# Performance work log

Hardware: AMD Instinct MI355X
Metric: run time of the kernel (lower is better)

The kernel has to match this reference:

```python
import jax, jax.numpy as jnp
import numpy as np

CHEB_K = 2  # Chebyshev polynomial order (init arg cheb_k)


def _avwgcn(x, E, w_pool, b_pool):
    """Adaptive Vertex-Wise Graph Convolution (AGCRN's AVWGCN).
    x: [B, N, C_in], E: [N, D], w_pool: [D, K, C_in, C_out], b_pool: [D, C_out].
    """
    N = E.shape[0]
    # adaptive adjacency from node embeddings
    supports = jax.nn.softmax(jax.nn.relu(E @ E.T), axis=1)  # [N, N]
    support_set = [jnp.eye(N, dtype=x.dtype), supports]
    for _ in range(2, CHEB_K):
        support_set.append(2.0 * supports @ support_set[-1] - support_set[-2])
    supports_k = jnp.stack(support_set)  # [K, N, N]
    # per-node adaptive weights/bias generated from embeddings
    weights = jnp.einsum('nd,dkio->nkio', E, w_pool)  # [N, K, C_in, C_out]
    bias = E @ b_pool  # [N, C_out]
    # graph propagation then per-node adaptive projection
    x_g = jnp.einsum('knm,bmc->bnkc', supports_k, x)  # [B, N, K, C_in]
    return jnp.einsum('bnki,nkio->bno', x_g, weights) + bias  # [B, N, C_out]


def setup_inputs() -> dict:
    key = jax.random.key(0)
    ks = jax.random.split(key, 7)
    B, N, DIN, DOUT, D = 64, 2048, 2, 64, 10
    return {
        'x': jax.random.normal(ks[0], (B, N, DIN), dtype=jnp.float32),
        'state': jax.random.normal(ks[1], (B, N, DOUT), dtype=jnp.float32),
        'node_embeddings': jax.random.normal(ks[2], (N, D), dtype=jnp.float32),
        'gate_w_pool': jax.random.normal(ks[3], (D, CHEB_K, DIN + DOUT, 2 * DOUT), dtype=jnp.float32) * 0.1,
        'gate_b_pool': jax.random.normal(ks[4], (D, 2 * DOUT), dtype=jnp.float32) * 0.1,
        'update_w_pool': jax.random.normal(ks[5], (D, CHEB_K, DIN + DOUT, DOUT), dtype=jnp.float32) * 0.1,
        'update_b_pool': jax.random.normal(ks[6], (D, DOUT), dtype=jnp.float32) * 0.1,
    }


def reference(x, state, node_embeddings, gate_w_pool, gate_b_pool, update_w_pool, update_b_pool):
    hidden_dim = state.shape[-1]
    input_and_state = jnp.concatenate([x, state], axis=-1)  # [B, N, DIN+DOUT]
    z_r = jax.nn.sigmoid(_avwgcn(input_and_state, node_embeddings, gate_w_pool, gate_b_pool))
    z, r = z_r[..., :hidden_dim], z_r[..., hidden_dim:]
    candidate = jnp.concatenate([x, z * state], axis=-1)
    hc = jnp.tanh(_avwgcn(candidate, node_embeddings, update_w_pool, update_b_pool))
    h = r * state + (1.0 - r) * hc
    return h
```

## Files before the change

### kernel.cpp

```cpp
#include <hip/hip_runtime.h>
#include <math.h>

#define N_NODES 2048
#define BATCH   64
#define DIN     2
#define DOUT    64
#define CIN     66
#define CP      68
#define D_EMB   10
#define GOUT    128
#define NCOLS   (BATCH*CP)
#define MK      2048
#define KTOT    132
#define KPAD    136

typedef __attribute__((ext_vector_type(8))) short bf16x8;
typedef __attribute__((ext_vector_type(8))) unsigned short u16x8;
typedef __attribute__((ext_vector_type(4))) float f32x4;

__device__ __forceinline__ unsigned short f2bf_rn(float f) {
    unsigned u = __builtin_bit_cast(unsigned, f);
    unsigned r = u + 0x7FFFu + ((u >> 16) & 1u);
    return (unsigned short)(r >> 16);
}
__device__ __forceinline__ float bf2f(unsigned short h) {
    unsigned u = ((unsigned)h) << 16;
    return __builtin_bit_cast(float, u);
}

__device__ __forceinline__ void gload_lds16(const void* g, void* l) {
    __builtin_amdgcn_global_load_lds(
        (const __attribute__((address_space(1))) unsigned int*)g,
        (__attribute__((address_space(3))) unsigned int*)l, 16, 0, 0);
}

__device__ __forceinline__ int frag_addr(int strip, int kt, int row, int slice) {
    const int byte = ((strip * 5 + kt) * 16 + row) * 64 + slice * 16;
    return byte ^ ((row & 7) << 4);
}

__global__ __launch_bounds__(256) void transpose_pool_kernel(
    const float* __restrict__ wp, float* __restrict__ wpT, int OC, int total)
{
    const int idx = blockIdx.x * 256 + threadIdx.x;
    if (idx >= total) return;
    const int kp   = idx % KPAD;
    const int rest = idx / KPAD;
    const int o    = rest % OC;
    const int d    = rest / OC;
    wpT[idx] = (kp < KTOT) ? wp[((size_t)d * KTOT + kp) * OC + o] : 0.f;
}

__global__ __launch_bounds__(256) void supports_kernel(
    const float* __restrict__ E, unsigned short* __restrict__ S_hi)
{
    const int n   = blockIdx.x;
    const int tid = threadIdx.x;

    float en[D_EMB];
#pragma unroll
    for (int d = 0; d < D_EMB; ++d) en[d] = E[n * D_EMB + d];

    float vals[8];
    float mx = -1e30f;
#pragma unroll
    for (int j = 0; j < 8; ++j) {
        const int m = tid + j * 256;
        float dot = 0.f;
#pragma unroll
        for (int d = 0; d < D_EMB; ++d) dot += en[d] * E[m * D_EMB + d];
        dot = fmaxf(dot, 0.f);
        vals[j] = dot;
        mx = fmaxf(mx, dot);
    }

    __shared__ float sred[4];
    for (int off = 32; off > 0; off >>= 1) mx = fmaxf(mx, __shfl_xor(mx, off));
    if ((tid & 63) == 0) sred[tid >> 6] = mx;
    __syncthreads();
    mx = fmaxf(fmaxf(sred[0], sred[1]), fmaxf(sred[2], sred[3]));

    float sum = 0.f;
#pragma unroll
    for (int j = 0; j < 8; ++j) { vals[j] = __expf(vals[j] - mx); sum += vals[j]; }

    __syncthreads();
    for (int off = 32; off > 0; off >>= 1) sum += __shfl_xor(sum, off);
    if ((tid & 63) == 0) sred[tid >> 6] = sum;
    __syncthreads();
    sum = sred[0] + sred[1] + sred[2] + sred[3];

    const float inv = 1.f / sum;
#pragma unroll
    for (int j = 0; j < 8; ++j)
        S_hi[(size_t)n * N_NODES + tid + j * 256] = f2bf_rn(vals[j] * inv);
}

__global__ __launch_bounds__(256) void build_xt_kernel(
    const float* __restrict__ x, const float* __restrict__ state,
    const unsigned short* __restrict__ zs, const int use_zs,
    unsigned short* __restrict__ XT)
{
    const int b   = blockIdx.y;
    const int m0  = blockIdx.x * 64;
    const int tid = threadIdx.x;
    __shared__ float T[64][69];

    {
        const int r = tid >> 2;
        const int q = (tid & 3) * 16;
        if (use_zs) {
            const u16x8 v0 = *(const u16x8*)&zs[((size_t)(m0 + r) * BATCH + b) * DOUT + q];
            const u16x8 v1 = *(const u16x8*)&zs[((size_t)(m0 + r) * BATCH + b) * DOUT + q + 8];
#pragma unroll
            for (int u = 0; u < 8; ++u) {
                T[r][DIN + q + u]     = bf2f(v0[u]);
                T[r][DIN + q + 8 + u] = bf2f(v1[u]);
            }
        } else {
#pragma unroll
            for (int u = 0; u < 4; ++u) {
                const float4 v = *(const float4*)&state[((size_t)b * N_NODES + m0 + r) * DOUT + q + u * 4];
                T[r][DIN + q + u * 4 + 0] = v.x;
                T[r][DIN + q + u * 4 + 1] = v.y;
                T[r][DIN + q + u * 4 + 2] = v.z;
                T[r][DIN + q + u * 4 + 3] = v.w;
            }
        }
    }
    if (tid < 128) {
        const int r = tid >> 1, c = tid & 1;
        T[r][c] = x[((size_t)b * N_NODES + m0 + r) * DIN + c];
        T[r][CIN + c] = 0.f;
    }
    __syncthreads();

    for (int idx = tid; idx < CP * 64; idx += 256) {
        const int c  = idx >> 6;
        const int mm = idx & 63;
        XT[((size_t)(b * CP + c)) * N_NODES + m0 + mm] = f2bf_rn(T[mm][c]);
    }
}

__global__ __launch_bounds__(256) void gemm_mfma_kernel(
    const unsigned short* __restrict__ A,
    const unsigned short* __restrict__ BT, float* __restrict__ C)
{
    __shared__ __align__(16) unsigned short As[4096];
    __shared__ __align__(16) unsigned short Bs[4096];

    const int tid  = threadIdx.x;
    const int lane = tid & 63;
    const int w    = tid >> 6;
    const int wr   = w >> 1, wc = w & 1;

    const int wg   = blockIdx.x;
    const int wgid = (wg & 7) * 68 + (wg >> 3);
    const int bn   = wgid % 34;
    const int bm   = wgid / 34;

    f32x4 acc[4][4];
#pragma unroll
    for (int i = 0; i < 4; ++i)
#pragma unroll
        for (int j = 0; j < 4; ++j) acc[i][j] = (f32x4){0.f, 0.f, 0.f, 0.f};

    const int srow = ((tid >> 6) << 4) + (tid & 15);
    const int scol = ((tid >> 4) & 3) * 8;
    const unsigned a_off0 = (unsigned)(bm * 128 + srow) * MK + scol;
    const unsigned a_off1 = a_off0 + 64u * MK;
    const unsigned b_off0 = (unsigned)(bn * 128 + srow) * MK + scol;
    const unsigned b_off1 = b_off0 + 64u * MK;

    unsigned short* asl0 = As + tid * 8;
    unsigned short* asl1 = As + 2048 + tid * 8;
    unsigned short* bsl0 = Bs + tid * 8;
    unsigned short* bsl1 = Bs + 2048 + tid * 8;

#pragma unroll 1
    for (int k0 = 0; k0 < MK; k0 += 32) {
        gload_lds16(A  + a_off0 + k0, asl0);
        gload_lds16(A  + a_off1 + k0, asl1);
        gload_lds16(BT + b_off0 + k0, bsl0);
        gload_lds16(BT + b_off1 + k0, bsl1);
        __syncthreads();

        bf16x8 af[4], bf[4];
#pragma unroll
        for (int i = 0; i < 4; ++i)
            af[i] = *(const bf16x8*)(As + ((wr * 4 + i) * 64 + lane) * 8);
#pragma unroll
        for (int j = 0; j < 4; ++j)
            bf[j] = *(const bf16x8*)(Bs + ((wc * 4 + j) * 64 + lane) * 8);
#pragma unroll
        for (int i = 0; i < 4; ++i)
#pragma unroll
            for (int j = 0; j < 4; ++j)
                acc[i][j] = __builtin_amdgcn_mfma_f32_16x16x32_bf16(
                    af[i], bf[j], acc[i][j], 0, 0, 0);
        __syncthreads();
    }

    const int crow0 = bm * 128 + wr * 64;
    const int ccol0 = bn * 128 + wc * 64;
#pragma unroll
    for (int i = 0; i < 4; ++i)
#pragma unroll
        for (int j = 0; j < 4; ++j)
#pragma unroll
            for (int r = 0; r < 4; ++r) {
                const int row = crow0 + i * 16 + (lane >> 4) * 4 + r;
                const int col = ccol0 + j * 16 + (lane & 15);
                C[(size_t)row * NCOLS + col] = acc[i][j][r];
            }
}

__global__ __launch_bounds__(256) void gate_mfma_kernel(
    const float* __restrict__ E, const float* __restrict__ wpT,
    const float* __restrict__ bp, const float* __restrict__ x,
    const float* __restrict__ state, const float* __restrict__ AG,
    unsigned short* __restrict__ ZS, float* __restrict__ Rbuf)
{
    const int n     = blockIdx.x;
    const int ohalf = blockIdx.y;
    const int tid   = threadIdx.x;

    __shared__ __align__(16) unsigned short INh[10240];
    __shared__ __align__(16) unsigned short Whi[10240];
    __shared__ __align__(16) unsigned short Wlo[10240];
    __shared__ float bias_l[64];

    float en[D_EMB];
#pragma unroll
    for (int d = 0; d < D_EMB; ++d) en[d] = E[n * D_EMB + d];

    for (int slot = tid; slot < 1280; slot += 256) {
        const int o = slot / 20, s = slot % 20;
        float v[8] = {0.f, 0.f, 0.f, 0.f, 0.f, 0.f, 0.f, 0.f};
        if (s < 17) {
            const float* p = wpT + ((size_t)(ohalf * 64 + o)) * KPAD + s * 8;
#pragma unroll
            for (int d = 0; d < D_EMB; ++d) {
                const float4 a = *(const float4*)(p + (size_t)d * GOUT * KPAD);
                const float4 b = *(const float4*)(p + (size_t)d * GOUT * KPAD + 4);
                v[0] += en[d] * a.x; v[1] += en[d] * a.y;
                v[2] += en[d] * a.z; v[3] += en[d] * a.w;
                v[4] += en[d] * b.x; v[5] += en[d] * b.y;
                v[6] += en[d] * b.z; v[7] += en[d] * b.w;
            }
        }
        u16x8 hv, lv;
#pragma unroll
        for (int u = 0; u < 8; ++u) {
            const unsigned short h = f2bf_rn(v[u]);
            hv[u] = h;
            lv[u] = f2bf_rn(v[u] - bf2f(h));
        }
        const int addr = frag_addr(o >> 4, s >> 2, o & 15, s & 3);
        *(u16x8*)((char*)Whi + addr) = hv;
        *(u16x8*)((char*)Wlo + addr) = lv;
    }
    if (tid < 64) {
        float s = 0.f;
#pragma unroll
        for (int d = 0; d < D_EMB; ++d) s += en[d] * bp[d * GOUT + ohalf * 64 + tid];
        bias_l[tid] = s;
    }
    for (int slot = tid; slot < 1280; slot += 256) {
        const int b = slot / 20, s = slot % 20;
        u16x8 hv;
#pragma unroll
        for (int u = 0; u < 8; ++u) {
            const int k = s * 8 + u;
            float v;
            if (k < DIN)       v = x[((size_t)b * N_NODES + n) * DIN + k];
            else if (k < CIN)  v = state[((size_t)b * N_NODES + n) * DOUT + k - DIN];
            else if (k < KTOT) v = AG[(size_t)n * NCOLS + b * CP + (k - CIN)];
            else               v = 0.f;
            hv[u] = f2bf_rn(v);
        }
        *(u16x8*)((char*)INh + frag_addr(b >> 4, s >> 2, b & 15, s & 3)) = hv;
    }
    __syncthreads();

    const int lane = tid & 63, w = tid >> 6;
    const int row = lane & 15, sl = lane >> 4;

    bf16x8 af[5];
#pragma unroll
    for (int kt = 0; kt < 5; ++kt)
        af[kt] = *(const bf16x8*)((const char*)INh + frag_addr(w, kt, row, sl));

    f32x4 acc[4];
#pragma unroll
    for (int j = 0; j < 4; ++j) acc[j] = (f32x4){0.f, 0.f, 0.f, 0.f};

#pragma unroll
    for (int j = 0; j < 4; ++j) {
#pragma unroll
        for (int kt = 0; kt < 5; ++kt) {
            const bf16x8 bh = *(const bf16x8*)((const char*)Whi + frag_addr(j, kt, row, sl));
            acc[j] = __builtin_amdgcn_mfma_f32_16x16x32_bf16(af[kt], bh, acc[j], 0, 0, 0);
        }
#pragma unroll
        for (int kt = 0; kt < 5; ++kt) {
            const bf16x8 bl = *(const bf16x8*)((const char*)Wlo + frag_addr(j, kt, row, sl));
            acc[j] = __builtin_amdgcn_mfma_f32_16x16x32_bf16(af[kt], bl, acc[j], 0, 0, 0);
        }
    }

#pragma unroll
    for (int j = 0; j < 4; ++j) {
        const int ol = j * 16 + row;
        const float bs = bias_l[ol];
#pragma unroll
        for (int r = 0; r < 4; ++r) {
            const int b = w * 16 + sl * 4 + r;
            const float sg = 1.f / (1.f + __expf(-(acc[j][r] + bs)));
            if (ohalf == 0) {
                ZS[((size_t)n * BATCH + b) * DOUT + ol] =
                    f2bf_rn(sg * state[((size_t)b * N_NODES + n) * DOUT + ol]);
            } else {
                Rbuf[((size_t)n * BATCH + b) * DOUT + ol] = sg;
            }
        }
    }
}

__global__ __launch_bounds__(256) void update_mfma_kernel(
    const float* __restrict__ E, const float* __restrict__ wpT,
    const float* __restrict__ bp, const float* __restrict__ x,
    const unsigned short* __restrict__ ZS, const float* __restrict__ AG,
    const float* __restrict__ state, const float* __restrict__ Rbuf,
    float* __restrict__ out)
{
    const int n   = blockIdx.x;
    const int tid = threadIdx.x;

    __shared__ __align__(16) unsigned short INh[10240];
    __shared__ __align__(16) unsigned short Whi[10240];
    __shared__ __align__(16) unsigned short Wlo[10240];
    __shared__ float bias_l[64];

    float en[D_EMB];
#pragma unroll
    for (int d = 0; d < D_EMB; ++d) en[d] = E[n * D_EMB + d];

    for (int slot = tid; slot < 1280; slot += 256) {
        const int o = slot / 20, s = slot % 20;
        float v[8] = {0.f, 0.f, 0.f, 0.f, 0.f, 0.f, 0.f, 0.f};
        if (s < 17) {
            const float* p = wpT + (size_t)o * KPAD + s * 8;
#pragma unroll
            for (int d = 0; d < D_EMB; ++d) {
                const float4 a = *(const float4*)(p + (size_t)d * DOUT * KPAD);
                const float4 b = *(const float4*)(p + (size_t)d * DOUT * KPAD + 4);
                v[0] += en[d] * a.x; v[1] += en[d] * a.y;
                v[2] += en[d] * a.z; v[3] += en[d] * a.w;
                v[4] += en[d] * b.x; v[5] += en[d] * b.y;
                v[6] += en[d] * b.z; v[7] += en[d] * b.w;
            }
        }
        u16x8 hv, lv;
#pragma unroll
        for (int u = 0; u < 8; ++u) {
            const unsigned short h = f2bf_rn(v[u]);
            hv[u] = h;
            lv[u] = f2bf_rn(v[u] - bf2f(h));
        }
        const int addr = frag_addr(o >> 4, s >> 2, o & 15, s & 3);
        *(u16x8*)((char*)Whi + addr) = hv;
        *(u16x8*)((char*)Wlo + addr) = lv;
    }
    if (tid < 64) {
        float s = 0.f;
#pragma unroll
        for (int d = 0; d < D_EMB; ++d) s += en[d] * bp[d * DOUT + tid];
        bias_l[tid] = s;
    }
    for (int slot = tid; slot < 1280; slot += 256) {
        const int b = slot / 20, s = slot % 20;
        u16x8 hv;
#pragma unroll
        for (int u = 0; u < 8; ++u) {
            const int k = s * 8 + u;
            float v;
            if (k < DIN)       v = x[((size_t)b * N_NODES + n) * DIN + k];
            else if (k < CIN)  v = bf2f(ZS[((size_t)n * BATCH + b) * DOUT + k - DIN]);
            else if (k < KTOT) v = AG[(size_t)n * NCOLS + b * CP + (k - CIN)];
            else               v = 0.f;
            hv[u] = f2bf_rn(v);
        }
        *(u16x8*)((char*)INh + frag_addr(b >> 4, s >> 2, b & 15, s & 3)) = hv;
    }
    __syncthreads();

    const int lane = tid & 63, w = tid >> 6;
    const int row = lane & 15, sl = lane >> 4;

    bf16x8 af[5];
#pragma unroll
    for (int kt = 0; kt < 5; ++kt)
        af[kt] = *(const bf16x8*)((const char*)INh + frag_addr(w, kt, row, sl));

    f32x4 acc[4];
#pragma unroll
    for (int j = 0; j < 4; ++j) acc[j] = (f32x4){0.f, 0.f, 0.f, 0.f};

#pragma unroll
    for (int j = 0; j < 4; ++j) {
#pragma unroll
        for (int kt = 0; kt < 5; ++kt) {
            const bf16x8 bh = *(const bf16x8*)((const char*)Whi + frag_addr(j, kt, row, sl));
            acc[j] = __builtin_amdgcn_mfma_f32_16x16x32_bf16(af[kt], bh, acc[j], 0, 0, 0);
        }
#pragma unroll
        for (int kt = 0; kt < 5; ++kt) {
            const bf16x8 bl = *(const bf16x8*)((const char*)Wlo + frag_addr(j, kt, row, sl));
            acc[j] = __builtin_amdgcn_mfma_f32_16x16x32_bf16(af[kt], bl, acc[j], 0, 0, 0);
        }
    }

#pragma unroll
    for (int j = 0; j < 4; ++j) {
        const int ol = j * 16 + row;
        const float bs = bias_l[ol];
#pragma unroll
        for (int r = 0; r < 4; ++r) {
            const int b = w * 16 + sl * 4 + r;
            const float hc = tanhf(acc[j][r] + bs);
            const float rr = Rbuf[((size_t)n * BATCH + b) * DOUT + ol];
            const float st = state[((size_t)b * N_NODES + n) * DOUT + ol];
            out[((size_t)b * N_NODES + n) * DOUT + ol] = rr * st + (1.f - rr) * hc;
        }
    }
}

extern "C" void kernel_launch(void* const* d_in, const int* in_sizes, int n_in,
                              void* d_out, int out_size, void* d_ws, size_t ws_size,
                              hipStream_t stream)
{
    const float* x  = (const float*)d_in[0];
    const float* st = (const float*)d_in[1];
    const float* E  = (const float*)d_in[2];
    const float* gw = (const float*)d_in[3];
    const float* gb = (const float*)d_in[4];
    const float* uw = (const float*)d_in[5];
    const float* ub = (const float*)d_in[6];
    float* out = (float*)d_out;

    unsigned short* S_hi = (unsigned short*)d_ws;
    unsigned short* XT   = S_hi + (size_t)N_NODES * N_NODES;
    float* AG = (float*)(XT + (size_t)NCOLS * N_NODES);
    unsigned short* ZS = (unsigned short*)(AG + (size_t)N_NODES * NCOLS);
    float* Rb   = (float*)(ZS + (size_t)N_NODES * BATCH * DOUT);
    float* wpTg = Rb + (size_t)N_NODES * BATCH * DOUT;
    float* wpTu = wpTg + (size_t)D_EMB * GOUT * KPAD;

    const int tg = D_EMB * GOUT * KPAD;
    const int tu = D_EMB * DOUT * KPAD;
    transpose_pool_kernel<<<(tg + 255) / 256, 256, 0, stream>>>(gw, wpTg, GOUT, tg);
    transpose_pool_kernel<<<(tu + 255) / 256, 256, 0, stream>>>(uw, wpTu, DOUT, tu);

    supports_kernel<<<N_NODES, 256, 0, stream>>>(E, S_hi);
    build_xt_kernel<<<dim3(N_NODES / 64, BATCH), 256, 0, stream>>>(x, st, ZS, 0, XT);
    gemm_mfma_kernel<<<544, 256, 0, stream>>>(S_hi, XT, AG);
    gate_mfma_kernel<<<dim3(N_NODES, 2), 256, 0, stream>>>(E, wpTg, gb, x, st, AG, ZS, Rb);
    build_xt_kernel<<<dim3(N_NODES / 64, BATCH), 256, 0, stream>>>(x, st, ZS, 1, XT);
    gemm_mfma_kernel<<<544, 256, 0, stream>>>(S_hi, XT, AG);
    update_mfma_kernel<<<N_NODES, 256, 0, stream>>>(E, wpTu, ub, x, ZS, AG, st, Rb, out);
}
```

Baseline: 538.8 us.

## Precompute per-node weights in separate kernel and write GEMM output as bf16 fragments

Per-node adaptive weight generation moves out of the gate and update kernels into a wgen kernel. It writes pre-swizzled hi/lo bf16 weight blobs, and the gate and update kernels load these straight into LDS with global_load_lds. The graph-propagation GEMM now writes bf16 directly into a unified per-(node, batch) input row layout that also holds z*state, replacing the fp32 AG buffer. The r gate is also stored as bf16. The aim is to cut redundant weight-generation work and memory traffic. The cost is extra launches, since the work is chunked by workspace size, and a round-trip of the weights through global memory.

Measured after the change: 485.4 us. 1.11x faster.

```diff
diff --git a/kernel.cpp b/kernel.cpp
--- a/kernel.cpp
+++ b/kernel.cpp
@@ -11,8 +11,10 @@
 #define GOUT    128
 #define NCOLS   (BATCH*CP)
 #define MK      2048
-#define KTOT    132
 #define KPAD    136
+#define INP     160
+#define WHALF   20480
+#define WBLOB   40960
 
 typedef __attribute__((ext_vector_type(8))) short bf16x8;
 typedef __attribute__((ext_vector_type(8))) unsigned short u16x8;
@@ -48,7 +50,7 @@
     const int rest = idx / KPAD;
     const int o    = rest % OC;
     const int d    = rest / OC;
-    wpT[idx] = (kp < KTOT) ? wp[((size_t)d * KTOT + kp) * OC + o] : 0.f;
+    wpT[idx] = (kp < 132) ? wp[((size_t)d * 132 + kp) * OC + o] : 0.f;
 }
 
 __global__ __launch_bounds__(256) void supports_kernel(
@@ -96,9 +98,17 @@
         S_hi[(size_t)n * N_NODES + tid + j * 256] = f2bf_rn(vals[j] * inv);
 }
 
+__global__ __launch_bounds__(256) void zero_tail_kernel(unsigned short* __restrict__ IN)
+{
+    const int idx = blockIdx.x * 256 + threadIdx.x;
+    if (idx >= N_NODES * BATCH * 13) return;
+    const int row = idx / 13, j = idx % 13;
+    *(unsigned int*)((char*)IN + (size_t)row * INP * 2 + 268 + j * 4) = 0u;
+}
+
 __global__ __launch_bounds__(256) void build_xt_kernel(
     const float* __restrict__ x, const float* __restrict__ state,
-    const unsigned short* __restrict__ zs, const int use_zs,
+    const unsigned short* __restrict__ INz, const int use_zs,
     unsigned short* __restrict__ XT)
 {
     const int b   = blockIdx.y;
@@ -110,12 +120,13 @@
         const int r = tid >> 2;
         const int q = (tid & 3) * 16;
         if (use_zs) {
-            const u16x8 v0 = *(const u16x8*)&zs[((size_t)(m0 + r) * BATCH + b) * DOUT + q];
-            const u16x8 v1 = *(const u16x8*)&zs[((size_t)(m0 + r) * BATCH + b) * DOUT + q + 8];
-#pragma unroll
-            for (int u = 0; u < 8; ++u) {
-                T[r][DIN + q + u]     = bf2f(v0[u]);
-                T[r][DIN + q + 8 + u] = bf2f(v1[u]);
+            const unsigned int* p = (const unsigned int*)
+                ((const char*)INz + (((size_t)(m0 + r) * BATCH + b) * INP + 2 + q) * 2);
+#pragma unroll
+            for (int t = 0; t < 8; ++t) {
+                const unsigned int v = p[t];
+                T[r][DIN + q + 2 * t]     = bf2f((unsigned short)(v & 0xFFFFu));
+                T[r][DIN + q + 2 * t + 1] = bf2f((unsigned short)(v >> 16));
             }
         } else {
 #pragma unroll
@@ -144,7 +155,7 @@
 
 __global__ __launch_bounds__(256) void gemm_mfma_kernel(
     const unsigned short* __restrict__ A,
-    const unsigned short* __restrict__ BT, float* __restrict__ C)
+    const unsigned short* __restrict__ BT, unsigned short* __restrict__ INout)
 {
     __shared__ __align__(16) unsigned short As[4096];
     __shared__ __align__(16) unsigned short Bs[4096];
@@ -204,50 +215,66 @@
     const int crow0 = bm * 128 + wr * 64;
     const int ccol0 = bn * 128 + wc * 64;
 #pragma unroll
-    for (int i = 0; i < 4; ++i)
-#pragma unroll
-        for (int j = 0; j < 4; ++j)
+    for (int j = 0; j < 4; ++j) {
+        const int col = ccol0 + j * 16 + (lane & 15);
+        const int b   = col / 68;
+        const int c   = col - b * 68;
+#pragma unroll
+        for (int i = 0; i < 4; ++i)
 #pragma unroll
             for (int r = 0; r < 4; ++r) {
                 const int row = crow0 + i * 16 + (lane >> 4) * 4 + r;
-                const int col = ccol0 + j * 16 + (lane & 15);
-                C[(size_t)row * NCOLS + col] = acc[i][j][r];
+                INout[((size_t)row * BATCH + b) * INP + 66 + c] = f2bf_rn(acc[i][j][r]);
             }
-}
-
-__global__ __launch_bounds__(256) void gate_mfma_kernel(
+    }
+}
+
+__global__ __launch_bounds__(256) void wgen_kernel(
     const float* __restrict__ E, const float* __restrict__ wpT,
-    const float* __restrict__ bp, const float* __restrict__ x,
-    const float* __restrict__ state, const float* __restrict__ AG,
-    unsigned short* __restrict__ ZS, float* __restrict__ Rbuf)
-{
-    const int n     = blockIdx.x;
-    const int ohalf = blockIdx.y;
-    const int tid   = threadIdx.x;
-
-    __shared__ __align__(16) unsigned short INh[10240];
-    __shared__ __align__(16) unsigned short Whi[10240];
-    __shared__ __align__(16) unsigned short Wlo[10240];
-    __shared__ float bias_l[64];
-
-    float en[D_EMB];
-#pragma unroll
-    for (int d = 0; d < D_EMB; ++d) en[d] = E[n * D_EMB + d];
-
-    for (int slot = tid; slot < 1280; slot += 256) {
-        const int o = slot / 20, s = slot % 20;
+    unsigned char* __restrict__ Wc, int n0, int NH, int OC)
+{
+    const int tid  = threadIdx.x;
+    const int cid  = blockIdx.x * 256 + tid;
+    const int half = cid / 1280;
+    const int rest = cid % 1280;
+    const int o_l  = rest / 20;
+    const int s    = rest % 20;
+    const int o_g  = half * 64 + o_l;
+
+    __shared__ float en_s[16][D_EMB];
+    if (tid < 16 * D_EMB) {
+        const int i = tid / D_EMB, d = tid % D_EMB;
+        en_s[i][d] = E[(n0 + blockIdx.y * 16 + i) * D_EMB + d];
+    }
+
+    float wv[D_EMB][8];
+    if (s < 17) {
+        const float* p = wpT + (size_t)o_g * KPAD + s * 8;
+#pragma unroll
+        for (int d = 0; d < D_EMB; ++d) {
+            const float4 a = *(const float4*)(p + (size_t)d * OC * KPAD);
+            const float4 b = *(const float4*)(p + (size_t)d * OC * KPAD + 4);
+            wv[d][0] = a.x; wv[d][1] = a.y; wv[d][2] = a.z; wv[d][3] = a.w;
+            wv[d][4] = b.x; wv[d][5] = b.y; wv[d][6] = b.z; wv[d][7] = b.w;
+        }
+    } else {
+#pragma unroll
+        for (int d = 0; d < D_EMB; ++d)
+#pragma unroll
+            for (int u = 0; u < 8; ++u) wv[d][u] = 0.f;
+    }
+    __syncthreads();
+
+    const int addr = frag_addr(o_l >> 4, s >> 2, o_l & 15, s & 3);
+    unsigned char* base0 = Wc + (size_t)blockIdx.y * 16 * NH * WBLOB + (size_t)half * WBLOB;
+#pragma unroll 1
+    for (int i = 0; i < 16; ++i) {
         float v[8] = {0.f, 0.f, 0.f, 0.f, 0.f, 0.f, 0.f, 0.f};
-        if (s < 17) {
-            const float* p = wpT + ((size_t)(ohalf * 64 + o)) * KPAD + s * 8;
-#pragma unroll
-            for (int d = 0; d < D_EMB; ++d) {
-                const float4 a = *(const float4*)(p + (size_t)d * GOUT * KPAD);
-                const float4 b = *(const float4*)(p + (size_t)d * GOUT * KPAD + 4);
-                v[0] += en[d] * a.x; v[1] += en[d] * a.y;
-                v[2] += en[d] * a.z; v[3] += en[d] * a.w;
-                v[4] += en[d] * b.x; v[5] += en[d] * b.y;
-                v[6] += en[d] * b.z; v[7] += en[d] * b.w;
-            }
+#pragma unroll
+        for (int d = 0; d < D_EMB; ++d) {
+            const float e = en_s[i][d];
+#pragma unroll
+            for (int u = 0; u < 8; ++u) v[u] += e * wv[d][u];
         }
         u16x8 hv, lv;
 #pragma unroll
@@ -256,182 +283,208 @@
             hv[u] = h;
             lv[u] = f2bf_rn(v[u] - bf2f(h));
         }
-        const int addr = frag_addr(o >> 4, s >> 2, o & 15, s & 3);
-        *(u16x8*)((char*)Whi + addr) = hv;
-        *(u16x8*)((char*)Wlo + addr) = lv;
-    }
+        unsigned char* nb = base0 + (size_t)i * NH * WBLOB;
+        *(u16x8*)(nb + addr)         = hv;
+        *(u16x8*)(nb + WHALF + addr) = lv;
+    }
+}
+
+union afrag { u16x8 u; bf16x8 s; };
+
+__global__ __launch_bounds__(256) void gate_mfma_kernel(
+    const float* __restrict__ E, const float* __restrict__ bp,
+    const float* __restrict__ x, const float* __restrict__ state,
+    unsigned short* __restrict__ IN, const unsigned char* __restrict__ Wc,
+    int n0, unsigned short* __restrict__ Rb)
+{
+    const int n_l  = blockIdx.x;
+    const int n    = n0 + n_l;
+    const int half = blockIdx.y;
+    const int tid  = threadIdx.x;
+
+    __shared__ __align__(16) unsigned char Ws[WBLOB];
+    __shared__ float bias_l[64];
+
+    const unsigned char* src = Wc + (size_t)n_l * (2 * WBLOB) + (size_t)half * WBLOB;
+#pragma unroll
+    for (int i = 0; i < 10; ++i)
+        gload_lds16(src + (tid + i * 256) * 16, Ws + (tid + i * 256) * 16);
+
     if (tid < 64) {
         float s = 0.f;
 #pragma unroll
-        for (int d = 0; d < D_EMB; ++d) s += en[d] * bp[d * GOUT + ohalf * 64 + tid];
+        for (int d = 0; d < D_EMB; ++d)
+            s += E[n * D_EMB + d] * bp[d * GOUT + half * 64 + tid];
         bias_l[tid] = s;
     }
-    for (int slot = tid; slot < 1280; slot += 256) {
-        const int b = slot / 20, s = slot % 20;
-        u16x8 hv;
-#pragma unroll
-        for (int u = 0; u < 8; ++u) {
-            const int k = s * 8 + u;
-            float v;
-            if (k < DIN)       v = x[((size_t)b * N_NODES + n) * DIN + k];
-            else if (k < CIN)  v = state[((size_t)b * N_NODES + n) * DOUT + k - DIN];
-            else if (k < KTOT) v = AG[(size_t)n * NCOLS + b * CP + (k - CIN)];
-            else               v = 0.f;
-            hv[u] = f2bf_rn(v);
-        }
-        *(u16x8*)((char*)INh + frag_addr(b >> 4, s >> 2, b & 15, s & 3)) = hv;
-    }
-    __syncthreads();
 
     const int lane = tid & 63, w = tid >> 6;
     const int row = lane & 15, sl = lane >> 4;
-
-    bf16x8 af[5];
-#pragma unroll
-    for (int kt = 0; kt < 5; ++kt)
-        af[kt] = *(const bf16x8*)((const char*)INh + frag_addr(w, kt, row, sl));
+    const int b = w * 16 + row;
+    const float* stp = state + ((size_t)b * N_NODES + n) * DOUT;
+    const float2 xv  = *(const float2*)(x + ((size_t)b * N_NODES + n) * DIN);
+    const unsigned short* inr = IN + ((size_t)n * BATCH + b) * INP;
+
+    afrag af[5];
+    {
+        float f[8];
+        if (sl == 0) {
+            f[0] = xv.x; f[1] = xv.y;
+            const float2 s0 = *(const float2*)(stp + 0);
+            const float2 s1 = *(const float2*)(stp + 2);
+            const float2 s2 = *(const float2*)(stp + 4);
+            f[2] = s0.x; f[3] = s0.y; f[4] = s1.x; f[5] = s1.y; f[6] = s2.x; f[7] = s2.y;
+        } else {
+            const float* sp = stp + sl * 8 - 2;
+#pragma unroll
+            for (int t = 0; t < 4; ++t) {
+                const float2 v = *(const float2*)(sp + 2 * t);
+                f[2 * t] = v.x; f[2 * t + 1] = v.y;
+            }
+        }
+#pragma unroll
+        for (int u = 0; u < 8; ++u) af[0].u[u] = f2bf_rn(f[u]);
+    }
+    {
+        const float* sp = stp + 30 + sl * 8;
+        float f[8];
+#pragma unroll
+        for (int t = 0; t < 4; ++t) {
+            const float2 v = *(const float2*)(sp + 2 * t);
+            f[2 * t] = v.x; f[2 * t + 1] = v.y;
+        }
+#pragma unroll
+        for (int u = 0; u < 8; ++u) af[1].u[u] = f2bf_rn(f[u]);
+    }
+    if (sl == 0) {
+        af[2].u[0] = f2bf_rn(stp[62]);
+        af[2].u[1] = f2bf_rn(stp[63]);
+        const unsigned int* q = (const unsigned int*)((const char*)inr + 132);
+        const unsigned int q0 = q[0], q1 = q[1], q2 = q[2];
+        af[2].u[2] = (unsigned short)q0; af[2].u[3] = (unsigned short)(q0 >> 16);
+        af[2].u[4] = (unsigned short)q1; af[2].u[5] = (unsigned short)(q1 >> 16);
+        af[2].u[6] = (unsigned short)q2; af[2].u[7] = (unsigned short)(q2 >> 16);
+    } else {
+        af[2].u = *(const u16x8*)(inr + 64 + sl * 8);
+    }
+    af[3].u = *(const u16x8*)(inr + 96 + sl * 8);
+    af[4].u = *(const u16x8*)(inr + 128 + sl * 8);
+
+    __syncthreads();
 
     f32x4 acc[4];
 #pragma unroll
     for (int j = 0; j < 4; ++j) acc[j] = (f32x4){0.f, 0.f, 0.f, 0.f};
-
 #pragma unroll
     for (int j = 0; j < 4; ++j) {
 #pragma unroll
         for (int kt = 0; kt < 5; ++kt) {
-            const bf16x8 bh = *(const bf16x8*)((const char*)Whi + frag_addr(j, kt, row, sl));
-            acc[j] = __builtin_amdgcn_mfma_f32_16x16x32_bf16(af[kt], bh, acc[j], 0, 0, 0);
+            const bf16x8 bh = *(const bf16x8*)(Ws + frag_addr(j, kt, row, sl));
+            acc[j] = __builtin_amdgcn_mfma_f32_16x16x32_bf16(af[kt].s, bh, acc[j], 0, 0, 0);
         }
 #pragma unroll
         for (int kt = 0; kt < 5; ++kt) {
-            const bf16x8 bl = *(const bf16x8*)((const char*)Wlo + frag_addr(j, kt, row, sl));
-            acc[j] = __builtin_amdgcn_mfma_f32_16x16x32_bf16(af[kt], bl, acc[j], 0, 0, 0);
+            const bf16x8 bl = *(const bf16x8*)(Ws + WHALF + frag_addr(j, kt, row, sl));
+            acc[j] = __builtin_amdgcn_mfma_f32_16x16x32_bf16(af[kt].s, bl, acc[j], 0, 0, 0);
         }
     }
 
 #pragma unroll
     for (int j = 0; j < 4; ++j) {
-        const int ol = j * 16 + row;
-        const float bs = bias_l[ol];
+        const int o_l = j * 16 + row;
+        const float bs = bias_l[o_l];
 #pragma unroll
         for (int r = 0; r < 4; ++r) {
-            const int b = w * 16 + sl * 4 + r;
+            const int bb = w * 16 + sl * 4 + r;
             const float sg = 1.f / (1.f + __expf(-(acc[j][r] + bs)));
-            if (ohalf == 0) {
-                ZS[((size_t)n * BATCH + b) * DOUT + ol] =
-                    f2bf_rn(sg * state[((size_t)b * N_NODES + n) * DOUT + ol]);
+            if (half == 0) {
+                const float st = state[((size_t)bb * N_NODES + n) * DOUT + o_l];
+                IN[((size_t)n * BATCH + bb) * INP + 2 + o_l] = f2bf_rn(sg * st);
             } else {
-                Rbuf[((size_t)n * BATCH + b) * DOUT + ol] = sg;
+                Rb[((size_t)n * BATCH + bb) * DOUT + o_l] = f2bf_rn(sg);
             }
         }
     }
 }
 
 __global__ __launch_bounds__(256) void update_mfma_kernel(
-    const float* __restrict__ E, const float* __restrict__ wpT,
-    const float* __restrict__ bp, const float* __restrict__ x,
-    const unsigned short* __restrict__ ZS, const float* __restrict__ AG,
-    const float* __restrict__ state, const float* __restrict__ Rbuf,
-    float* __restrict__ out)
-{
-    const int n   = blockIdx.x;
+    const float* __restrict__ E, const float* __restrict__ bp,
+    const float* __restrict__ x, const float* __restrict__ state,
+    const unsigned short* __restrict__ IN, const unsigned char* __restrict__ Wc,
+    int n0, const unsigned short* __restrict__ Rb, float* __restrict__ out)
+{
+    const int n_l = blockIdx.x;
+    const int n   = n0 + n_l;
     const int tid = threadIdx.x;
 
-    __shared__ __align__(16) unsigned short INh[10240];
-    __shared__ __align__(16) unsigned short Whi[10240];
-    __shared__ __align__(16) unsigned short Wlo[10240];
+    __shared__ __align__(16) unsigned char Ws[WBLOB];
     __shared__ float bias_l[64];
 
-    float en[D_EMB];
-#pragma unroll
-    for (int d = 0; d < D_EMB; ++d) en[d] = E[n * D_EMB + d];
-
-    for (int slot = tid; slot < 1280; slot += 256) {
-        const int o = slot / 20, s = slot % 20;
-        float v[8] = {0.f, 0.f, 0.f, 0.f, 0.f, 0.f, 0.f, 0.f};
-        if (s < 17) {
-            const float* p = wpT + (size_t)o * KPAD + s * 8;
-#pragma unroll
-            for (int d = 0; d < D_EMB; ++d) {
-                const float4 a = *(const float4*)(p + (size_t)d * DOUT * KPAD);
-                const float4 b = *(const float4*)(p + (size_t)d * DOUT * KPAD + 4);
-                v[0] += en[d] * a.x; v[1] += en[d] * a.y;
-                v[2] += en[d] * a.z; v[3] += en[d] * a.w;
-                v[4] += en[d] * b.x; v[5] += en[d] * b.y;
-                v[6] += en[d] * b.z; v[7] += en[d] * b.w;
-            }
-        }
-        u16x8 hv, lv;
-#pragma unroll
-        for (int u = 0; u < 8; ++u) {
-            const unsigned short h = f2bf_rn(v[u]);
-            hv[u] = h;
-            lv[u] = f2bf_rn(v[u] - bf2f(h));
-        }
-        const int addr = frag_addr(o >> 4, s >> 2, o & 15, s & 3);
-        *(u16x8*)((char*)Whi + addr) = hv;
-        *(u16x8*)((char*)Wlo + addr) = lv;
-    }
+    const unsigned char* src = Wc + (size_t)n_l * WBLOB;
+#pragma unroll
+    for (int i = 0; i < 10; ++i)
+        gload_lds16(src + (tid + i * 256) * 16, Ws + (tid + i * 256) * 16);
+
     if (tid < 64) {
         float s = 0.f;
 #pragma unroll
-        for (int d = 0; d < D_EMB; ++d) s += en[d] * bp[d * DOUT + tid];
+        for (int d = 0; d < D_EMB; ++d)
+            s += E[n * D_EMB + d] * bp[d * DOUT + tid];
         bias_l[tid] = s;
     }
-    for (int slot = tid; slot < 1280; slot += 256) {
-        const int b = slot / 20, s = slot % 20;
-        u16x8 hv;
-#pragma unroll
-        for (int u = 0; u < 8; ++u) {
-            const int k = s * 8 + u;
-            float v;
-            if (k < DIN)       v = x[((size_t)b * N_NODES + n) * DIN + k];
-            else if (k < CIN)  v = bf2f(ZS[((size_t)n * BATCH + b) * DOUT + k - DIN]);
-            else if (k < KTOT) v = AG[(size_t)n * NCOLS + b * CP + (k - CIN)];
-            else               v = 0.f;
-            hv[u] = f2bf_rn(v);
-        }
-        *(u16x8*)((char*)INh + frag_addr(b >> 4, s >> 2, b & 15, s & 3)) = hv;
-    }
-    __syncthreads();
 
     const int lane = tid & 63, w = tid >> 6;
     const int row = lane & 15, sl = lane >> 4;
-
-    bf16x8 af[5];
-#pragma unroll
-    for (int kt = 0; kt < 5; ++kt)
-        af[kt] = *(const bf16x8*)((const char*)INh + frag_addr(w, kt, row, sl));
+    const int b = w * 16 + row;
+    const unsigned short* inr = IN + ((size_t)n * BATCH + b) * INP;
+
+    afrag af[5];
+    if (sl == 0) {
+        const float2 xv = *(const float2*)(x + ((size_t)b * N_NODES + n) * DIN);
+        af[0].u[0] = f2bf_rn(xv.x);
+        af[0].u[1] = f2bf_rn(xv.y);
+        const unsigned int* q = (const unsigned int*)((const char*)inr + 4);
+        const unsigned int q0 = q[0], q1 = q[1], q2 = q[2];
+        af[0].u[2] = (unsigned short)q0; af[0].u[3] = (unsigned short)(q0 >> 16);
+        af[0].u[4] = (unsigned short)q1; af[0].u[5] = (unsigned short)(q1 >> 16);
+        af[0].u[6] = (unsigned short)q2; af[0].u[7] = (unsigned short)(q2 >> 16);
+    } else {
+        af[0].u = *(const u16x8*)(inr + sl * 8);
+    }
+#pragma unroll
+    for (int kt = 1; kt < 5; ++kt)
+        af[kt].u = *(const u16x8*)(inr + kt * 32 + sl * 8);
+
+    __syncthreads();
 
     f32x4 acc[4];
 #pragma unroll
     for (int j = 0; j < 4; ++j) acc[j] = (f32x4){0.f, 0.f, 0.f, 0.f};
-
 #pragma unroll
     for (int j = 0; j < 4; ++j) {
 #pragma unroll
         for (int kt = 0; kt < 5; ++kt) {
-            const bf16x8 bh = *(const bf16x8*)((const char*)Whi + frag_addr(j, kt, row, sl));
-            acc[j] = __builtin_amdgcn_mfma_f32_16x16x32_bf16(af[kt], bh, acc[j], 0, 0, 0);
+            const bf16x8 bh = *(const bf16x8*)(Ws + frag_addr(j, kt, row, sl));
+            acc[j] = __builtin_amdgcn_mfma_f32_16x16x32_bf16(af[kt].s, bh, acc[j], 0, 0, 0);
         }
 #pragma unroll
         for (int kt = 0; kt < 5; ++kt) {
-            const bf16x8 bl = *(const bf16x8*)((const char*)Wlo + frag_addr(j, kt, row, sl));
-            acc[j] = __builtin_amdgcn_mfma_f32_16x16x32_bf16(af[kt], bl, acc[j], 0, 0, 0);
+            const bf16x8 bl = *(const bf16x8*)(Ws + WHALF + frag_addr(j, kt, row, sl));
+            acc[j] = __builtin_amdgcn_mfma_f32_16x16x32_bf16(af[kt].s, bl, acc[j], 0, 0, 0);
         }
     }
 
 #pragma unroll
     for (int j = 0; j < 4; ++j) {
-        const int ol = j * 16 + row;
-        const float bs = bias_l[ol];
+        const int o_l = j * 16 + row;
+        const float bs = bias_l[o_l];
 #pragma unroll
         for (int r = 0; r < 4; ++r) {
-            const int b = w * 16 + sl * 4 + r;
+            const int bb = w * 16 + sl * 4 + r;
             const float hc = tanhf(acc[j][r] + bs);
-            const float rr = Rbuf[((size_t)n * BATCH + b) * DOUT + ol];
-            const float st = state[((size_t)b * N_NODES + n) * DOUT + ol];
-            out[((size_t)b * N_NODES + n) * DOUT + ol] = rr * st + (1.f - rr) * hc;
+            const float rr = bf2f(Rb[((size_t)n * BATCH + bb) * DOUT + o_l]);
+            const float st = state[((size_t)bb * N_NODES + n) * DOUT + o_l];
+            out[((size_t)bb * N_NODES + n) * DOUT + o_l] = rr * st + (1.f - rr) * hc;
         }
     }
 }
@@ -449,13 +502,22 @@
     const float* ub = (const float*)d_in[6];
     float* out = (float*)d_out;
 
-    unsigned short* S_hi = (unsigned short*)d_ws;
-    unsigned short* XT   = S_hi + (size_t)N_NODES * N_NODES;
-    float* AG = (float*)(XT + (size_t)NCOLS * N_NODES);
-    unsigned short* ZS = (unsigned short*)(AG + (size_t)N_NODES * NCOLS);
-    float* Rb   = (float*)(ZS + (size_t)N_NODES * BATCH * DOUT);
-    float* wpTg = Rb + (size_t)N_NODES * BATCH * DOUT;
-    float* wpTu = wpTg + (size_t)D_EMB * GOUT * KPAD;
+    unsigned char* ws = (unsigned char*)d_ws;
+    unsigned short* S_hi = (unsigned short*)ws;
+    unsigned short* XT   = (unsigned short*)(ws + 8388608);
+    unsigned short* IN   = (unsigned short*)(ws + 26214400);
+    unsigned short* Rb   = (unsigned short*)(ws + 68157440);
+    float* wpTg          = (float*)(ws + 84934656);
+    float* wpTu          = (float*)(ws + 85630976);
+    unsigned char* Wc    = ws + 85979136;
+
+    const size_t fixed_b = 85979136;
+    int C = 64;
+    const int cands[5] = {2048, 1024, 512, 256, 128};
+    for (int i = 0; i < 5; ++i) {
+        if (ws_size >= fixed_b + (size_t)cands[i] * (2 * WBLOB)) { C = cands[i]; break; }
+    }
+    const int nch = N_NODES / C;
 
     const int tg = D_EMB * GOUT * KPAD;
     const int tu = D_EMB * DOUT * KPAD;
@@ -463,10 +525,22 @@
     transpose_pool_kernel<<<(tu + 255) / 256, 256, 0, stream>>>(uw, wpTu, DOUT, tu);
 
     supports_kernel<<<N_NODES, 256, 0, stream>>>(E, S_hi);
-    build_xt_kernel<<<dim3(N_NODES / 64, BATCH), 256, 0, stream>>>(x, st, ZS, 0, XT);
-    gemm_mfma_kernel<<<544, 256, 0, stream>>>(S_hi, XT, AG);
-    gate_mfma_kernel<<<dim3(N_NODES, 2), 256, 0, stream>>>(E, wpTg, gb, x, st, AG, ZS, Rb);
-    build_xt_kernel<<<dim3(N_NODES / 64, BATCH), 256, 0, stream>>>(x, st, ZS, 1, XT);
-    gemm_mfma_kernel<<<544, 256, 0, stream>>>(S_hi, XT, AG);
-    update_mfma_kernel<<<N_NODES, 256, 0, stream>>>(E, wpTu, ub, x, ZS, AG, st, Rb, out);
-}
+    zero_tail_kernel<<<(N_NODES * BATCH * 13 + 255) / 256, 256, 0, stream>>>(IN);
+    build_xt_kernel<<<dim3(N_NODES / 64, BATCH), 256, 0, stream>>>(x, st, IN, 0, XT);
+    gemm_mfma_kernel<<<544, 256, 0, stream>>>(S_hi, XT, IN);
+
+    for (int ch = 0; ch < nch; ++ch) {
+        const int n0 = ch * C;
+        wgen_kernel<<<dim3(10, C / 16), 256, 0, stream>>>(E, wpTg, Wc, n0, 2, GOUT);
+        gate_mfma_kernel<<<dim3(C, 2), 256, 0, stream>>>(E, gb, x, st, IN, Wc, n0, Rb);
+    }
+
+    build_xt_kernel<<<dim3(N_NODES / 64, BATCH), 256, 0, stream>>>(x, st, IN, 1, XT);
+    gemm_mfma_kernel<<<544, 256, 0, stream>>>(S_hi, XT, IN);
+
+    for (int ch = 0; ch < nch; ++ch) {
+        const int n0 = ch * C;
+        wgen_kernel<<<dim3(5, C / 16), 256, 0, stream>>>(E, wpTu, Wc, n0, 1, DOUT);
+        update_mfma_kernel<<<C, 256, 0, stream>>>(E, ub, x, st, IN, Wc, n0, Rb, out);
+    }
+}
```
